# Kernel tuning notes

Measured on AMD Instinct MI355X. Metric: run time of the kernel, lower is better.

Reference implementation:

```python
import jax, jax.numpy as jnp
import numpy as np

B, H, N, E = 16, 8, 2048, 64
D = 64          # dpb dim
PD = D // 4     # pos_dim = d // 4


def _ln(x, g, b):
    m = jnp.mean(x, axis=-1, keepdims=True)
    v = jnp.var(x, axis=-1, keepdims=True)
    return (x - m) / jnp.sqrt(v + 1e-5) * g + b


def _dpb(t, w0, b0, g1, gb1, w1, b1, g2, gb2, w2, b2, g3, gb3, w3, b3):
    # DynamicPosBias (non-residual): pos3(pos2(pos1(proj(t))))
    h = t @ w0 + b0                               # [m, PD]
    h = jax.nn.relu(_ln(h, g1, gb1)) @ w1 + b1    # [m, PD]
    h = jax.nn.relu(_ln(h, g2, gb2)) @ w2 + b2    # [m, PD]
    return jax.nn.relu(_ln(h, g3, gb3)) @ w3 + b3 # [m, H]


def setup_inputs():
    key = jax.random.key(0)
    ks = jax.random.split(key, 8)
    s = 0.02
    return {
        'x': jax.random.normal(ks[0], (B, H, N, E), jnp.float32),
        'gamma': jnp.ones((1,), jnp.float32) * 10.0,
        'w0': jax.random.normal(ks[1], (1, PD), jnp.float32) * s,
        'b0': jnp.zeros((PD,), jnp.float32),
        'ln1_g': jnp.ones((PD,), jnp.float32), 'ln1_b': jnp.zeros((PD,), jnp.float32),
        'w1': jax.random.normal(ks[2], (PD, PD), jnp.float32) * s,
        'b1': jnp.zeros((PD,), jnp.float32),
        'ln2_g': jnp.ones((PD,), jnp.float32), 'ln2_b': jnp.zeros((PD,), jnp.float32),
        'w2': jax.random.normal(ks[3], (PD, PD), jnp.float32) * s,
        'b2': jnp.zeros((PD,), jnp.float32),
        'ln3_g': jnp.ones((PD,), jnp.float32), 'ln3_b': jnp.zeros((PD,), jnp.float32),
        'w3': jax.random.normal(ks[4], (PD, H), jnp.float32) * s,
        'b3': jnp.zeros((H,), jnp.float32),
    }


def reference(x, gamma, w0, b0, ln1_g, ln1_b, w1, b1, ln2_g, ln2_b, w2, b2, ln3_g, ln3_b, w3, b3):
    n = x.shape[-2]  # n == self.n, so l1 = n-1, l2 = 0
    dpb = lambda t: _dpb(t, w0, b0, ln1_g, ln1_b, w1, b1, ln2_g, ln2_b, w2, b2, ln3_g, ln3_b, w3, b3)
    pos_t = jnp.arange(1, n, dtype=x.dtype)[:, None]          # self.pos[:l1] == self.pos[-l1:]
    pd = dpb(pos_t).T                                         # [H, n-1]
    pos_dpb, neg_dpb = pd, pd                                 # non-causal, same inputs
    zero_dpb = dpb(jnp.zeros((1, 1), x.dtype)).T              # [H, 1]
    # decay (use_decay=True, use_exp=True): additive log-sigmoid decay
    coef = jnp.arange(1, n, dtype=x.dtype)[None]              # [1, n-1]
    glog = jnp.log(jax.nn.sigmoid(gamma)) * coef
    pos = glog + pos_dpb
    neg = jnp.flip(glog, axis=1) + neg_dpb
    a = jnp.exp(jnp.clip(jnp.concatenate([zero_dpb, pos, zero_dpb, neg], axis=-1), -60.0, 30.0))  # [H, 2n]
    # FFT Toeplitz conv
    y = jnp.fft.rfft(x, 2 * n, axis=-2, norm='ortho')         # [B, H, n+1, E] complex
    v = jnp.fft.rfft(a, axis=1)[None, :, :, None]             # [1, H, n+1, 1]
    out = jnp.fft.irfft(v * y, 2 * n, axis=-2, norm='ortho')[:, :, :n, :]
    return out
```

## Files before the change

### kernel.cpp

```cpp
#include <hip/hip_runtime.h>
#include <math.h>

#define NPOS 2048
#define MFFT 4096
#define NH 8
#define PDW 16
#define NE 64
#define NB 16

#define PP(i) ((i) + ((i) >> 4))
#define SH_SZ (MFFT + MFFT / 16)

__device__ __forceinline__ float2 cmul(float2 a, float2 b) {
    return make_float2(a.x * b.x - a.y * b.y, a.x * b.y + a.y * b.x);
}

template <int NT>
__device__ void fft_fwd(float2* sh, int tid) {
    #pragma unroll
    for (int st = 0; st < 6; ++st) {
        const int logL = 12 - 2 * st;
        const int logQ = logL - 2;
        const int Q = 1 << logQ;
        const float cmag = -6.283185307179586f / (float)(1 << logL);
        __syncthreads();
        #pragma unroll
        for (int kk = 0; kk < 1024 / NT; ++kk) {
            int m = tid + kk * NT;
            int t = m & (Q - 1);
            int base = ((m >> logQ) << logL) + t;
            float2 x0 = sh[PP(base)];
            float2 x1 = sh[PP(base + Q)];
            float2 x2 = sh[PP(base + 2 * Q)];
            float2 x3 = sh[PP(base + 3 * Q)];
            float2 s02 = make_float2(x0.x + x2.x, x0.y + x2.y);
            float2 d02 = make_float2(x0.x - x2.x, x0.y - x2.y);
            float2 s13 = make_float2(x1.x + x3.x, x1.y + x3.y);
            float2 d13 = make_float2(x1.x - x3.x, x1.y - x3.y);
            float2 y0 = make_float2(s02.x + s13.x, s02.y + s13.y);
            float2 y2 = make_float2(s02.x - s13.x, s02.y - s13.y);
            float2 y1 = make_float2(d02.x + d13.y, d02.y - d13.x);
            float2 y3 = make_float2(d02.x - d13.y, d02.y + d13.x);
            float sn, cs;
            __sincosf(cmag * (float)t, &sn, &cs);
            float2 w1 = make_float2(cs, sn);
            float2 w2 = cmul(w1, w1);
            float2 w3 = cmul(w2, w1);
            sh[PP(base)]         = y0;
            sh[PP(base + Q)]     = cmul(y1, w1);
            sh[PP(base + 2 * Q)] = cmul(y2, w2);
            sh[PP(base + 3 * Q)] = cmul(y3, w3);
        }
    }
}

template <int NT>
__device__ void fft_inv(float2* sh, int tid) {
    #pragma unroll
    for (int st = 0; st < 6; ++st) {
        const int logL = 2 + 2 * st;
        const int logQ = logL - 2;
        const int Q = 1 << logQ;
        const float cmag = 6.283185307179586f / (float)(1 << logL);
        __syncthreads();
        #pragma unroll
        for (int kk = 0; kk < 1024 / NT; ++kk) {
            int m = tid + kk * NT;
            int t = m & (Q - 1);
            int base = ((m >> logQ) << logL) + t;
            float2 z0 = sh[PP(base)];
            float2 z1 = sh[PP(base + Q)];
            float2 z2 = sh[PP(base + 2 * Q)];
            float2 z3 = sh[PP(base + 3 * Q)];
            float sn, cs;
            __sincosf(cmag * (float)t, &sn, &cs);
            float2 w1 = make_float2(cs, sn);
            float2 w2 = cmul(w1, w1);
            float2 w3 = cmul(w2, w1);
            float2 u0 = z0;
            float2 u1 = cmul(z1, w1);
            float2 u2 = cmul(z2, w2);
            float2 u3 = cmul(z3, w3);
            float2 s02 = make_float2(u0.x + u2.x, u0.y + u2.y);
            float2 d02 = make_float2(u0.x - u2.x, u0.y - u2.y);
            float2 s13 = make_float2(u1.x + u3.x, u1.y + u3.y);
            float2 d13 = make_float2(u1.x - u3.x, u1.y - u3.y);
            sh[PP(base)]         = make_float2(s02.x + s13.x, s02.y + s13.y);
            sh[PP(base + 2 * Q)] = make_float2(s02.x - s13.x, s02.y - s13.y);
            sh[PP(base + Q)]     = make_float2(d02.x - d13.y, d02.y + d13.x);
            sh[PP(base + 3 * Q)] = make_float2(d02.x + d13.y, d02.y - d13.x);
        }
    }
}

#define LN_RELU(G, Bv)                                                        \
    {                                                                         \
        float mu = 0.f;                                                       \
        _Pragma("unroll") for (int i = 0; i < PDW; ++i) mu += h[i];           \
        mu *= (1.0f / PDW);                                                   \
        float var = 0.f;                                                      \
        _Pragma("unroll") for (int i = 0; i < PDW; ++i) {                     \
            float d = h[i] - mu;                                              \
            var += d * d;                                                     \
        }                                                                     \
        var *= (1.0f / PDW);                                                  \
        float inv = 1.0f / sqrtf(var + 1e-5f);                                \
        _Pragma("unroll") for (int i = 0; i < PDW; ++i) {                     \
            float nv = (h[i] - mu) * inv * G[i] + Bv[i];                      \
            r[i] = fmaxf(nv, 0.f);                                            \
        }                                                                     \
    }

__global__ __launch_bounds__(256) void dpb_mlp_kernel(
    const float* __restrict__ w0, const float* __restrict__ b0,
    const float* __restrict__ g1, const float* __restrict__ gb1,
    const float* __restrict__ w1, const float* __restrict__ b1,
    const float* __restrict__ g2, const float* __restrict__ gb2,
    const float* __restrict__ w2, const float* __restrict__ b2,
    const float* __restrict__ g3, const float* __restrict__ gb3,
    const float* __restrict__ w3, const float* __restrict__ b3,
    float* __restrict__ dpbout)
{
    int p = blockIdx.x * 256 + threadIdx.x;
    if (p >= NPOS) return;
    float t = (float)p;
    float h[PDW], r[PDW];
    #pragma unroll
    for (int i = 0; i < PDW; ++i) h[i] = t * w0[i] + b0[i];

    LN_RELU(g1, gb1);
    #pragma unroll
    for (int j = 0; j < PDW; ++j) {
        float acc = b1[j];
        #pragma unroll
        for (int i = 0; i < PDW; ++i) acc += r[i] * w1[i * PDW + j];
        h[j] = acc;
    }
    LN_RELU(g2, gb2);
    #pragma unroll
    for (int j = 0; j < PDW; ++j) {
        float acc = b2[j];
        #pragma unroll
        for (int i = 0; i < PDW; ++i) acc += r[i] * w2[i * PDW + j];
        h[j] = acc;
    }
    LN_RELU(g3, gb3);
    #pragma unroll
    for (int hh = 0; hh < NH; ++hh) {
        float acc = b3[hh];
        #pragma unroll
        for (int i = 0; i < PDW; ++i) acc += r[i] * w3[i * NH + hh];
        dpbout[p * NH + hh] = acc;
    }
}

__global__ __launch_bounds__(1024) void toeplitz_fft_kernel(
    const float* __restrict__ gamma, const float* __restrict__ dpbout,
    float2* __restrict__ V)
{
    __shared__ float2 sh[SH_SZ];
    int h = blockIdx.x;
    int tid = threadIdx.x;
    float g = gamma[0];
    float lsg = -log1pf(expf(-g));
    #pragma unroll
    for (int j = 0; j < 4; ++j) {
        int k = tid + (j << 10);
        float val;
        if (k == 0 || k == NPOS) val = dpbout[h];
        else if (k < NPOS)       val = lsg * (float)k + dpbout[k * NH + h];
        else                     val = lsg * (float)(2 * NPOS - k) + dpbout[(k - NPOS) * NH + h];
        val = fminf(30.f, fmaxf(-60.f, val));
        sh[PP(k)] = make_float2(expf(val) * (1.0f / (float)MFFT), 0.f);
    }
    fft_fwd<1024>(sh, tid);
    __syncthreads();
    #pragma unroll
    for (int j = 0; j < 4; ++j) {
        int k = tid + (j << 10);
        V[h * MFFT + k] = sh[PP(k)];
    }
}

__global__ __launch_bounds__(512) void conv_kernel(
    const float* __restrict__ x, const float2* __restrict__ V,
    float* __restrict__ out)
{
    __shared__ float2 sh[SH_SZ];
    int wg = blockIdx.x;
    int xcd = wg & 7;
    int slot = wg >> 3;
    int pair = slot & 31;
    int bh = ((slot >> 5) << 3) | xcd;
    int h = bh & (NH - 1);
    int tid = threadIdx.x;

    const float* xp = x + (size_t)bh * NPOS * NE + pair * 2;
    #pragma unroll
    for (int j = 0; j < 4; ++j) {
        int s = tid + (j << 9);
        sh[PP(s)] = *reinterpret_cast<const float2*>(xp + (size_t)s * NE);
    }
    #pragma unroll
    for (int j = 4; j < 8; ++j) sh[PP(tid + (j << 9))] = make_float2(0.f, 0.f);

    fft_fwd<512>(sh, tid);
    __syncthreads();

    const float2* Vh = V + h * MFFT;
    #pragma unroll
    for (int j = 0; j < 8; ++j) {
        int k = tid + (j << 9);
        sh[PP(k)] = cmul(sh[PP(k)], Vh[k]);
    }

    fft_inv<512>(sh, tid);
    __syncthreads();

    float* op = out + (size_t)bh * NPOS * NE + pair * 2;
    #pragma unroll
    for (int j = 0; j < 4; ++j) {
        int s = tid + (j << 9);
        *reinterpret_cast<float2*>(op + (size_t)s * NE) = sh[PP(s)];
    }
}

extern "C" void kernel_launch(void* const* d_in, const int* in_sizes, int n_in,
                              void* d_out, int out_size, void* d_ws, size_t ws_size,
                              hipStream_t stream) {
    const float* x     = (const float*)d_in[0];
    const float* gamma = (const float*)d_in[1];
    const float* w0    = (const float*)d_in[2];
    const float* b0    = (const float*)d_in[3];
    const float* g1    = (const float*)d_in[4];
    const float* gb1   = (const float*)d_in[5];
    const float* w1    = (const float*)d_in[6];
    const float* b1    = (const float*)d_in[7];
    const float* g2    = (const float*)d_in[8];
    const float* gb2   = (const float*)d_in[9];
    const float* w2    = (const float*)d_in[10];
    const float* b2    = (const float*)d_in[11];
    const float* g3    = (const float*)d_in[12];
    const float* gb3   = (const float*)d_in[13];
    const float* w3    = (const float*)d_in[14];
    const float* b3    = (const float*)d_in[15];
    float* out = (float*)d_out;

    float*  dpbout = (float*)d_ws;
    float2* V      = (float2*)((char*)d_ws + 65536);

    dpb_mlp_kernel<<<NPOS / 256, 256, 0, stream>>>(w0, b0, g1, gb1, w1, b1,
                                                   g2, gb2, w2, b2, g3, gb3,
                                                   w3, b3, dpbout);
    toeplitz_fft_kernel<<<NH, 1024, 0, stream>>>(gamma, dpbout, V);
    conv_kernel<<<NB * NH * 32, 512, 0, stream>>>(x, V, out);
}
```

Baseline: 261.2 us.

## Replace radix-4 shared-memory FFT with register-resident radix-8 Stockham-style FFT

Rewrites the 4096-point FFTs as four radix-8 passes that keep eight values in registers per thread and go through shared memory only between passes, using an XOR swizzle instead of padding. This cuts shared-memory round trips and barriers from six radix-4 stages to three exchanges. The forward transform exploits the zero-padded upper half of the input, and the inverse skips computing the discarded outputs. The frequency-domain multiply is fused in registers with vectorized spectrum loads in a digit-reversed order that matches between the forward and inverse transforms. The DPB MLP now uses one thread per (position, head) pair, and the spectrum kernel uses 512 threads.

```diff
diff --git a/kernel.cpp b/kernel.cpp
--- a/kernel.cpp
+++ b/kernel.cpp
@@ -8,89 +8,103 @@
 #define NE 64
 #define NB 16
 
-#define PP(i) ((i) + ((i) >> 4))
-#define SH_SZ (MFFT + MFFT / 16)
-
 __device__ __forceinline__ float2 cmul(float2 a, float2 b) {
     return make_float2(a.x * b.x - a.y * b.y, a.x * b.y + a.y * b.x);
 }
-
-template <int NT>
-__device__ void fft_fwd(float2* sh, int tid) {
-    #pragma unroll
-    for (int st = 0; st < 6; ++st) {
-        const int logL = 12 - 2 * st;
-        const int logQ = logL - 2;
-        const int Q = 1 << logQ;
-        const float cmag = -6.283185307179586f / (float)(1 << logL);
-        __syncthreads();
-        #pragma unroll
-        for (int kk = 0; kk < 1024 / NT; ++kk) {
-            int m = tid + kk * NT;
-            int t = m & (Q - 1);
-            int base = ((m >> logQ) << logL) + t;
-            float2 x0 = sh[PP(base)];
-            float2 x1 = sh[PP(base + Q)];
-            float2 x2 = sh[PP(base + 2 * Q)];
-            float2 x3 = sh[PP(base + 3 * Q)];
-            float2 s02 = make_float2(x0.x + x2.x, x0.y + x2.y);
-            float2 d02 = make_float2(x0.x - x2.x, x0.y - x2.y);
-            float2 s13 = make_float2(x1.x + x3.x, x1.y + x3.y);
-            float2 d13 = make_float2(x1.x - x3.x, x1.y - x3.y);
-            float2 y0 = make_float2(s02.x + s13.x, s02.y + s13.y);
-            float2 y2 = make_float2(s02.x - s13.x, s02.y - s13.y);
-            float2 y1 = make_float2(d02.x + d13.y, d02.y - d13.x);
-            float2 y3 = make_float2(d02.x - d13.y, d02.y + d13.x);
-            float sn, cs;
-            __sincosf(cmag * (float)t, &sn, &cs);
-            float2 w1 = make_float2(cs, sn);
-            float2 w2 = cmul(w1, w1);
-            float2 w3 = cmul(w2, w1);
-            sh[PP(base)]         = y0;
-            sh[PP(base + Q)]     = cmul(y1, w1);
-            sh[PP(base + 2 * Q)] = cmul(y2, w2);
-            sh[PP(base + 3 * Q)] = cmul(y3, w3);
-        }
-    }
-}
-
-template <int NT>
-__device__ void fft_inv(float2* sh, int tid) {
-    #pragma unroll
-    for (int st = 0; st < 6; ++st) {
-        const int logL = 2 + 2 * st;
-        const int logQ = logL - 2;
-        const int Q = 1 << logQ;
-        const float cmag = 6.283185307179586f / (float)(1 << logL);
-        __syncthreads();
-        #pragma unroll
-        for (int kk = 0; kk < 1024 / NT; ++kk) {
-            int m = tid + kk * NT;
-            int t = m & (Q - 1);
-            int base = ((m >> logQ) << logL) + t;
-            float2 z0 = sh[PP(base)];
-            float2 z1 = sh[PP(base + Q)];
-            float2 z2 = sh[PP(base + 2 * Q)];
-            float2 z3 = sh[PP(base + 3 * Q)];
-            float sn, cs;
-            __sincosf(cmag * (float)t, &sn, &cs);
-            float2 w1 = make_float2(cs, sn);
-            float2 w2 = cmul(w1, w1);
-            float2 w3 = cmul(w2, w1);
-            float2 u0 = z0;
-            float2 u1 = cmul(z1, w1);
-            float2 u2 = cmul(z2, w2);
-            float2 u3 = cmul(z3, w3);
-            float2 s02 = make_float2(u0.x + u2.x, u0.y + u2.y);
-            float2 d02 = make_float2(u0.x - u2.x, u0.y - u2.y);
-            float2 s13 = make_float2(u1.x + u3.x, u1.y + u3.y);
-            float2 d13 = make_float2(u1.x - u3.x, u1.y - u3.y);
-            sh[PP(base)]         = make_float2(s02.x + s13.x, s02.y + s13.y);
-            sh[PP(base + 2 * Q)] = make_float2(s02.x - s13.x, s02.y - s13.y);
-            sh[PP(base + Q)]     = make_float2(d02.x - d13.y, d02.y + d13.x);
-            sh[PP(base + 3 * Q)] = make_float2(d02.x + d13.y, d02.y - d13.x);
-        }
-    }
+__device__ __forceinline__ float2 f2add(float2 a, float2 b) {
+    return make_float2(a.x + b.x, a.y + b.y);
+}
+__device__ __forceinline__ float2 f2sub(float2 a, float2 b) {
+    return make_float2(a.x - b.x, a.y - b.y);
+}
+
+__device__ __forceinline__ int swz(int a) {
+    return a ^ ((a >> 3) & 7) ^ (((a >> 6) & 7) << 3);
+}
+
+template <int SGN, int MODE>
+__device__ __forceinline__ void dft8(float2 v[8]) {
+    const float c = 0.70710678118654757f;
+    float2 E0, E1, E2, E3, O0, O1, O2, O3;
+    if (MODE == 1) {
+        float2 a = v[0], b = v[2];
+        E0 = f2add(a, b); E2 = f2sub(a, b);
+        E1 = (SGN < 0) ? make_float2(a.x + b.y, a.y - b.x) : make_float2(a.x - b.y, a.y + b.x);
+        E3 = (SGN < 0) ? make_float2(a.x - b.y, a.y + b.x) : make_float2(a.x + b.y, a.y - b.x);
+        a = v[1]; b = v[3];
+        O0 = f2add(a, b); O2 = f2sub(a, b);
+        O1 = (SGN < 0) ? make_float2(a.x + b.y, a.y - b.x) : make_float2(a.x - b.y, a.y + b.x);
+        O3 = (SGN < 0) ? make_float2(a.x - b.y, a.y + b.x) : make_float2(a.x + b.y, a.y - b.x);
+    } else {
+        float2 t0 = f2add(v[0], v[4]), t1 = f2sub(v[0], v[4]);
+        float2 t2 = f2add(v[2], v[6]), t3 = f2sub(v[2], v[6]);
+        E0 = f2add(t0, t2); E2 = f2sub(t0, t2);
+        E1 = (SGN < 0) ? make_float2(t1.x + t3.y, t1.y - t3.x) : make_float2(t1.x - t3.y, t1.y + t3.x);
+        E3 = (SGN < 0) ? make_float2(t1.x - t3.y, t1.y + t3.x) : make_float2(t1.x + t3.y, t1.y - t3.x);
+        t0 = f2add(v[1], v[5]); t1 = f2sub(v[1], v[5]);
+        t2 = f2add(v[3], v[7]); t3 = f2sub(v[3], v[7]);
+        O0 = f2add(t0, t2); O2 = f2sub(t0, t2);
+        O1 = (SGN < 0) ? make_float2(t1.x + t3.y, t1.y - t3.x) : make_float2(t1.x - t3.y, t1.y + t3.x);
+        O3 = (SGN < 0) ? make_float2(t1.x - t3.y, t1.y + t3.x) : make_float2(t1.x + t3.y, t1.y - t3.x);
+    }
+    float2 w1O, w2O, w3O;
+    if (SGN < 0) {
+        w1O = make_float2(c * (O1.x + O1.y), c * (O1.y - O1.x));
+        w2O = make_float2(O2.y, -O2.x);
+        w3O = make_float2(c * (O3.y - O3.x), -c * (O3.x + O3.y));
+    } else {
+        w1O = make_float2(c * (O1.x - O1.y), c * (O1.y + O1.x));
+        w2O = make_float2(-O2.y, O2.x);
+        w3O = make_float2(-c * (O3.x + O3.y), c * (O3.x - O3.y));
+    }
+    v[0] = f2add(E0, O0); v[1] = f2add(E1, w1O);
+    v[2] = f2add(E2, w2O); v[3] = f2add(E3, w3O);
+    if (MODE != 2) {
+        v[4] = f2sub(E0, O0); v[5] = f2sub(E1, w1O);
+        v[6] = f2sub(E2, w2O); v[7] = f2sub(E3, w3O);
+    }
+}
+
+__device__ __forceinline__ void twiddle8(float2 u[8], float ang) {
+    float2 w1; __sincosf(ang, &w1.y, &w1.x);
+    float2 w2 = cmul(w1, w1), w3 = cmul(w1, w2), w4 = cmul(w2, w2);
+    float2 w5 = cmul(w2, w3), w6 = cmul(w3, w3), w7 = cmul(w3, w4);
+    u[1] = cmul(u[1], w1); u[2] = cmul(u[2], w2); u[3] = cmul(u[3], w3);
+    u[4] = cmul(u[4], w4); u[5] = cmul(u[5], w5); u[6] = cmul(u[6], w6);
+    u[7] = cmul(u[7], w7);
+}
+
+#define A4096 1.5339807878856412e-3f
+#define A512  1.2271846303085130e-2f
+#define A64   9.8174770424681035e-2f
+
+template <int MODE1>
+__device__ __forceinline__ void fftR8_fwd(float2 v[8], float2* sh, int m) {
+    dft8<-1, MODE1>(v);
+    twiddle8(v, -A4096 * (float)m);
+    #pragma unroll
+    for (int j = 0; j < 8; ++j) sh[swz(m + 512 * j)] = v[j];
+    __syncthreads();
+    int t2 = m & 63, b2 = (m >> 6) << 9;
+    #pragma unroll
+    for (int r = 0; r < 8; ++r) v[r] = sh[swz(b2 + t2 + 64 * r)];
+    dft8<-1, 0>(v);
+    twiddle8(v, -A512 * (float)t2);
+    #pragma unroll
+    for (int j = 0; j < 8; ++j) sh[swz(b2 + t2 + 64 * j)] = v[j];
+    __syncthreads();
+    int t3 = m & 7, b3 = (m >> 3) << 6;
+    #pragma unroll
+    for (int r = 0; r < 8; ++r) v[r] = sh[swz(b3 + t3 + 8 * r)];
+    dft8<-1, 0>(v);
+    twiddle8(v, -A64 * (float)t3);
+    #pragma unroll
+    for (int j = 0; j < 8; ++j) sh[swz(b3 + t3 + 8 * j)] = v[j];
+    __syncthreads();
+    int b4 = m << 3;
+    #pragma unroll
+    for (int r = 0; r < 8; ++r) v[r] = sh[swz(b4 + r)];
+    dft8<-1, 0>(v);
 }
 
 #define LN_RELU(G, Bv)                                                        \
@@ -121,13 +135,12 @@
     const float* __restrict__ w3, const float* __restrict__ b3,
     float* __restrict__ dpbout)
 {
-    int p = blockIdx.x * 256 + threadIdx.x;
-    if (p >= NPOS) return;
-    float t = (float)p;
+    int idx = blockIdx.x * 256 + threadIdx.x;
+    int hh = idx & 7;
+    float t = (float)(idx >> 3);
     float h[PDW], r[PDW];
     #pragma unroll
     for (int i = 0; i < PDW; ++i) h[i] = t * w0[i] + b0[i];
-
     LN_RELU(g1, gb1);
     #pragma unroll
     for (int j = 0; j < PDW; ++j) {
@@ -145,84 +158,97 @@
         h[j] = acc;
     }
     LN_RELU(g3, gb3);
-    #pragma unroll
-    for (int hh = 0; hh < NH; ++hh) {
-        float acc = b3[hh];
-        #pragma unroll
-        for (int i = 0; i < PDW; ++i) acc += r[i] * w3[i * NH + hh];
-        dpbout[p * NH + hh] = acc;
-    }
-}
-
-__global__ __launch_bounds__(1024) void toeplitz_fft_kernel(
+    float acc = b3[hh];
+    #pragma unroll
+    for (int i = 0; i < PDW; ++i) acc += r[i] * w3[i * NH + hh];
+    dpbout[idx] = acc;
+}
+
+__global__ __launch_bounds__(512) void toeplitz_fft_kernel(
     const float* __restrict__ gamma, const float* __restrict__ dpbout,
     float2* __restrict__ V)
 {
-    __shared__ float2 sh[SH_SZ];
-    int h = blockIdx.x;
-    int tid = threadIdx.x;
-    float g = gamma[0];
-    float lsg = -log1pf(expf(-g));
-    #pragma unroll
-    for (int j = 0; j < 4; ++j) {
-        int k = tid + (j << 10);
+    __shared__ float2 sh[MFFT];
+    int hh = blockIdx.x;
+    int m = threadIdx.x;
+    float lsg = -log1pf(__expf(-gamma[0]));
+    float2 v[8];
+    #pragma unroll
+    for (int r = 0; r < 8; ++r) {
+        int k = m + 512 * r;
         float val;
-        if (k == 0 || k == NPOS) val = dpbout[h];
-        else if (k < NPOS)       val = lsg * (float)k + dpbout[k * NH + h];
-        else                     val = lsg * (float)(2 * NPOS - k) + dpbout[(k - NPOS) * NH + h];
+        if (k == 0 || k == NPOS)  val = dpbout[hh];
+        else if (k < NPOS)        val = lsg * (float)k + dpbout[k * NH + hh];
+        else                      val = lsg * (float)(2 * NPOS - k) + dpbout[(k - NPOS) * NH + hh];
         val = fminf(30.f, fmaxf(-60.f, val));
-        sh[PP(k)] = make_float2(expf(val) * (1.0f / (float)MFFT), 0.f);
-    }
-    fft_fwd<1024>(sh, tid);
-    __syncthreads();
-    #pragma unroll
-    for (int j = 0; j < 4; ++j) {
-        int k = tid + (j << 10);
-        V[h * MFFT + k] = sh[PP(k)];
-    }
+        v[r] = make_float2(__expf(val) * (1.0f / (float)MFFT), 0.f);
+    }
+    fftR8_fwd<0>(v, sh, m);
+    #pragma unroll
+    for (int j = 0; j < 8; ++j) V[hh * MFFT + 8 * m + j] = v[j];
 }
 
 __global__ __launch_bounds__(512) void conv_kernel(
     const float* __restrict__ x, const float2* __restrict__ V,
     float* __restrict__ out)
 {
-    __shared__ float2 sh[SH_SZ];
+    __shared__ float2 sh[MFFT];
     int wg = blockIdx.x;
     int xcd = wg & 7;
     int slot = wg >> 3;
     int pair = slot & 31;
     int bh = ((slot >> 5) << 3) | xcd;
     int h = bh & (NH - 1);
-    int tid = threadIdx.x;
+    int m = threadIdx.x;
 
     const float* xp = x + (size_t)bh * NPOS * NE + pair * 2;
-    #pragma unroll
-    for (int j = 0; j < 4; ++j) {
-        int s = tid + (j << 9);
-        sh[PP(s)] = *reinterpret_cast<const float2*>(xp + (size_t)s * NE);
-    }
-    #pragma unroll
-    for (int j = 4; j < 8; ++j) sh[PP(tid + (j << 9))] = make_float2(0.f, 0.f);
-
-    fft_fwd<512>(sh, tid);
-    __syncthreads();
-
-    const float2* Vh = V + h * MFFT;
-    #pragma unroll
-    for (int j = 0; j < 8; ++j) {
-        int k = tid + (j << 9);
-        sh[PP(k)] = cmul(sh[PP(k)], Vh[k]);
-    }
-
-    fft_inv<512>(sh, tid);
-    __syncthreads();
+    float2 v[8];
+    #pragma unroll
+    for (int r = 0; r < 4; ++r)
+        v[r] = *reinterpret_cast<const float2*>(xp + (size_t)(m + 512 * r) * NE);
+    #pragma unroll
+    for (int r = 4; r < 8; ++r) v[r] = make_float2(0.f, 0.f);
+
+    fftR8_fwd<1>(v, sh, m);
+
+    int b4 = m << 3;
+    const float4* V4 = reinterpret_cast<const float4*>(V + h * MFFT + b4);
+    #pragma unroll
+    for (int j2 = 0; j2 < 4; ++j2) {
+        float4 f = V4[j2];
+        v[2 * j2]     = cmul(v[2 * j2],     make_float2(f.x, f.y));
+        v[2 * j2 + 1] = cmul(v[2 * j2 + 1], make_float2(f.z, f.w));
+    }
+
+    dft8<1, 0>(v);
+    #pragma unroll
+    for (int r = 0; r < 8; ++r) sh[swz(b4 + r)] = v[r];
+    __syncthreads();
+    int t3 = m & 7, b3 = (m >> 3) << 6;
+    #pragma unroll
+    for (int j = 0; j < 8; ++j) v[j] = sh[swz(b3 + t3 + 8 * j)];
+    twiddle8(v, A64 * (float)t3);
+    dft8<1, 0>(v);
+    #pragma unroll
+    for (int r = 0; r < 8; ++r) sh[swz(b3 + t3 + 8 * r)] = v[r];
+    __syncthreads();
+    int t2 = m & 63, b2 = (m >> 6) << 9;
+    #pragma unroll
+    for (int j = 0; j < 8; ++j) v[j] = sh[swz(b2 + t2 + 64 * j)];
+    twiddle8(v, A512 * (float)t2);
+    dft8<1, 0>(v);
+    #pragma unroll
+    for (int r = 0; r < 8; ++r) sh[swz(b2 + t2 + 64 * r)] = v[r];
+    __syncthreads();
+    #pragma unroll
+    for (int j = 0; j < 8; ++j) v[j] = sh[swz(m + 512 * j)];
+    twiddle8(v, A4096 * (float)m);
+    dft8<1, 2>(v);
 
     float* op = out + (size_t)bh * NPOS * NE + pair * 2;
     #pragma unroll
-    for (int j = 0; j < 4; ++j) {
-        int s = tid + (j << 9);
-        *reinterpret_cast<float2*>(op + (size_t)s * NE) = sh[PP(s)];
-    }
+    for (int r = 0; r < 4; ++r)
+        *reinterpret_cast<float2*>(op + (size_t)(m + 512 * r) * NE) = v[r];
 }
 
 extern "C" void kernel_launch(void* const* d_in, const int* in_sizes, int n_in,
@@ -249,9 +275,9 @@
     float*  dpbout = (float*)d_ws;
     float2* V      = (float2*)((char*)d_ws + 65536);
 
-    dpb_mlp_kernel<<<NPOS / 256, 256, 0, stream>>>(w0, b0, g1, gb1, w1, b1,
-                                                   g2, gb2, w2, b2, g3, gb3,
-                                                   w3, b3, dpbout);
-    toeplitz_fft_kernel<<<NH, 1024, 0, stream>>>(gamma, dpbout, V);
+    dpb_mlp_kernel<<<NPOS * NH / 256, 256, 0, stream>>>(w0, b0, g1, gb1, w1, b1,
+                                                        g2, gb2, w2, b2, g3, gb3,
+                                                        w3, b3, dpbout);
+    toeplitz_fft_kernel<<<NH, 512, 0, stream>>>(gamma, dpbout, V);
     conv_kernel<<<NB * NH * 32, 512, 0, stream>>>(x, V, out);
 }
```

Measured after the change: 230.5 us. 1.13x faster.
